# Optimization experiments

Hardware: AMD Instinct MI355X
Metric: run time of the kernel (lower is better)

Reference implementation:

```python
import jax, jax.numpy as jnp
import numpy as np

DIM = 2048
N_HEADS = 16
Q_RANK = 1536
KV_RANK = 512
D_NOPE = 128
D_ROPE = 64
D_V = 128
EPS = 1e-6
B, S = 2, 2048
ROPE_THETA = 10000.0


def rmsnorm(x, w, eps=EPS):
    return x * jax.lax.rsqrt(jnp.mean(x * x, axis=-1, keepdims=True) + eps) * w


def apply_rope(x):
    # x: [b, h, s, d] with d even; LLaMA-style interleaved pair rotation
    b, h, s, d = x.shape
    inv_freq = 1.0 / (ROPE_THETA ** (jnp.arange(0, d, 2, dtype=jnp.float32) / d))
    ang = jnp.arange(s, dtype=jnp.float32)[:, None] * inv_freq[None, :]  # [s, d/2]
    cos, sin = jnp.cos(ang), jnp.sin(ang)
    xr = x.reshape(b, h, s, d // 2, 2)
    x1, x2 = xr[..., 0], xr[..., 1]
    o1 = x1 * cos - x2 * sin
    o2 = x1 * sin + x2 * cos
    return jnp.stack([o1, o2], axis=-1).reshape(b, h, s, d)


def setup_inputs() -> dict:
    key = jax.random.key(0)
    ks = jax.random.split(key, 10)
    std = 0.02
    return {
        "x": jax.random.normal(ks[0], (B, S, DIM), dtype=jnp.float32),
        "wq_down": jax.random.normal(ks[1], (Q_RANK, DIM), dtype=jnp.float32) * std,
        "q_norm_w": jnp.ones((Q_RANK,), dtype=jnp.float32),
        "wq_up": jax.random.normal(ks[2], (N_HEADS * D_NOPE, Q_RANK), dtype=jnp.float32) * std,
        "wq_rope": jax.random.normal(ks[3], (N_HEADS * D_ROPE, Q_RANK), dtype=jnp.float32) * std,
        "wkv_down": jax.random.normal(ks[4], (KV_RANK, DIM), dtype=jnp.float32) * std,
        "kv_norm_w": jnp.ones((KV_RANK,), dtype=jnp.float32),
        "wkv_up": jax.random.normal(ks[5], (N_HEADS * (D_NOPE + D_V), KV_RANK), dtype=jnp.float32) * std,
        "wk_rope": jax.random.normal(ks[6], (D_ROPE, DIM), dtype=jnp.float32) * std,
        "wo": jax.random.normal(ks[7], (DIM, N_HEADS * D_V), dtype=jnp.float32) * std,
    }


def reference(x, wq_down, q_norm_w, wq_up, wq_rope, wkv_down, kv_norm_w, wkv_up, wk_rope, wo):
    bs, s, _ = x.shape
    # low-rank Q path
    q_c = rmsnorm(x @ wq_down.T, q_norm_w)                              # [b,s,qr]
    q_nope = (q_c @ wq_up.T).reshape(bs, s, N_HEADS, D_NOPE).transpose(0, 2, 1, 3)
    q_pe = (q_c @ wq_rope.T).reshape(bs, s, N_HEADS, D_ROPE).transpose(0, 2, 1, 3)
    # low-rank KV path
    kv_c = rmsnorm(x @ wkv_down.T, kv_norm_w)                           # [b,s,kvr]
    kv_up = (kv_c @ wkv_up.T).reshape(bs, s, N_HEADS, D_NOPE + D_V)
    k_nope = kv_up[..., :D_NOPE].transpose(0, 2, 1, 3)                  # [b,h,s,dn]
    v = kv_up[..., D_NOPE:].transpose(0, 2, 1, 3)                       # [b,h,s,dv]
    # shared rope key (1 head), broadcast across heads
    k_rope = (x @ wk_rope.T).reshape(bs, s, 1, D_ROPE).transpose(0, 2, 1, 3)  # [b,1,s,dr]
    q_pe = apply_rope(q_pe)
    k_rope = apply_rope(k_rope)
    q = jnp.concatenate([q_nope, q_pe], axis=-1)                        # [b,h,s,dn+dr]
    k = jnp.concatenate([k_nope, jnp.broadcast_to(k_rope, (bs, N_HEADS, s, D_ROPE))], axis=-1)
    scale = 1.0 / np.sqrt(D_NOPE + D_ROPE)
    scores = jnp.einsum('bhqd,bhkd->bhqk', q, k) * scale                # [b,h,s,s]
    causal = jnp.tril(jnp.ones((s, s), dtype=bool))
    scores = jnp.where(causal, scores, -jnp.inf)
    probs = jax.nn.softmax(scores, axis=-1)
    out = jnp.einsum('bhqk,bhkv->bhqv', probs, v)                       # [b,h,s,dv]
    out = out.transpose(0, 2, 1, 3).reshape(bs, s, N_HEADS * D_V)
    return out @ wo.T
```

## Files before the change

### kernel.cpp

```cpp
#include <hip/hip_runtime.h>
#include <stdint.h>

typedef _Float16 f16x8 __attribute__((ext_vector_type(8)));
typedef _Float16 f16x4 __attribute__((ext_vector_type(4)));
typedef float fx4 __attribute__((ext_vector_type(4)));

static constexpr int S_LEN = 2048;
static constexpr int BATCH = 2;
static constexpr int TOKENS = BATCH * S_LEN;
static constexpr int DIM = 2048;
static constexpr int NH = 16;
static constexpr int QR = 1536;
static constexpr int KVR = 512;
static constexpr int DN = 128;
static constexpr int DR = 64;
static constexpr int DV = 128;

__device__ __forceinline__ void async16(const _Float16* g, _Float16* lds_base_uniform) {
  __builtin_amdgcn_global_load_lds(
      (const __attribute__((address_space(1))) void*)g,
      (__attribute__((address_space(3))) void*)lds_base_uniform, 16, 0, 0);
}

__device__ __forceinline__ void bar() {
  asm volatile("" ::: "memory");
  __builtin_amdgcn_s_barrier();
  asm volatile("" ::: "memory");
}
#define VMWAIT(n) asm volatile("s_waitcnt vmcnt(" #n ")" ::: "memory")

#define ROR16(x, ctrl) \
  __uint_as_float(__builtin_amdgcn_update_dpp(__float_as_uint(x), __float_as_uint(x), \
                                              (ctrl), 0xF, 0xF, false))

__device__ __forceinline__ void sincos_rev(float ang, float* sn, float* cs) {
  float rev = ang * 0.15915494309189535f;
  rev -= floorf(rev);
  *sn = __builtin_amdgcn_sinf(rev);
  *cs = __builtin_amdgcn_cosf(rev);
}

struct CvtSegs {
  const float* src[8];
  _Float16* dst[8];
  int n4[8];
  int cum[9];
};
__global__ __launch_bounds__(256) void cvt_all(CvtSegs s) {
  const int b = blockIdx.x;
  int seg = 0;
#pragma unroll
  for (int k = 0; k < 7; ++k) seg += (b >= s.cum[seg + 1]) ? 1 : 0;
  const int i = (b - s.cum[seg]) * 256 + threadIdx.x;
  if (i >= s.n4[seg]) return;
  fx4 v = *(const fx4*)(s.src[seg] + (size_t)i * 4);
  f16x4 o;
  o[0] = (_Float16)v[0]; o[1] = (_Float16)v[1];
  o[2] = (_Float16)v[2]; o[3] = (_Float16)v[3];
  *(f16x4*)(s.dst[seg] + (size_t)i * 4) = o;
}

template <int MODE>
__global__ __launch_bounds__(256) void gemm_nt(const _Float16* __restrict__ A,
                                               const _Float16* __restrict__ W,
                                               void* __restrict__ C0v,
                                               void* __restrict__ C1v,
                                               void* __restrict__ C2v,
                                               int M, int N, int K) {
  __shared__ __attribute__((aligned(16))) _Float16 As[3][128 * 32];
  __shared__ __attribute__((aligned(16))) _Float16 Ws[3][128 * 32];
  const int tid = threadIdx.x;
  const int lane = tid & 63;
  const int wave = tid >> 6;
  const int wr = (wave >> 1) * 64;
  const int wc = (wave & 1) * 64;
  const int m16 = lane & 15;
  const int quad = lane >> 4;
  const int m0 = blockIdx.y * 128;
  const int n0 = blockIdx.x * 128;

  auto stage = [&](int buf, int k0) {
#pragma unroll
    for (int p = 0; p < 2; ++p) {
      const int cb = p * 256 + wave * 64;
      const int ch = cb + lane;
      const int r = ch >> 2;
      const int c8 = (ch & 3) * 8;
      async16(A + (size_t)(m0 + r) * K + k0 + c8, &As[buf][cb * 8]);
      async16(W + (size_t)(n0 + r) * K + k0 + c8, &Ws[buf][cb * 8]);
    }
  };

  const fx4 fz = {0.f, 0.f, 0.f, 0.f};
  fx4 acc[4][4];
#pragma unroll
  for (int i = 0; i < 4; ++i)
#pragma unroll
    for (int j = 0; j < 4; ++j) acc[i][j] = fz;

  const int nkt = K >> 5;
  stage(0, 0);
  stage(1, 32);
  int cur = 0;
  for (int kt = 0; kt < nkt; ++kt) {
    if (kt + 1 < nkt) { VMWAIT(4); } else { VMWAIT(0); }
    bar();
    if (kt + 2 < nkt) {
      int b2 = cur + 2; if (b2 >= 3) b2 -= 3;
      stage(b2, (kt + 2) * 32);
    }
    const _Float16* as = As[cur];
    const _Float16* ws = Ws[cur];
    f16x8 af[4], wf[4];
#pragma unroll
    for (int i = 0; i < 4; ++i)
      af[i] = *(const f16x8*)(&as[(wr + i * 16 + m16) * 32 + quad * 8]);
#pragma unroll
    for (int j = 0; j < 4; ++j)
      wf[j] = *(const f16x8*)(&ws[(wc + j * 16 + m16) * 32 + quad * 8]);
#pragma unroll
    for (int i = 0; i < 4; ++i)
#pragma unroll
      for (int j = 0; j < 4; ++j)
        acc[i][j] = __builtin_amdgcn_mfma_f32_16x16x32_f16(af[i], wf[j], acc[i][j], 0, 0, 0);
    if (++cur == 3) cur = 0;
  }

#pragma unroll
  for (int j = 0; j < 4; ++j) {
    const int col = n0 + wc + j * 16 + m16;
    if (MODE == 5) {
#pragma unroll
      for (int i = 0; i < 4; ++i)
#pragma unroll
        for (int r = 0; r < 4; ++r) {
          const size_t row = (size_t)(m0 + wr + i * 16 + quad * 4 + r);
          const _Float16 v = (_Float16)acc[i][j][r];
          if (col < 1536)      ((_Float16*)C0v)[row * 1536 + col] = v;
          else if (col < 2048) ((_Float16*)C1v)[row * 512 + col - 1536] = v;
          else if (col < 2112) ((_Float16*)C2v)[row * 64 + col - 2048] = v;
        }
    } else {
      if (col < N) {
#pragma unroll
        for (int i = 0; i < 4; ++i)
#pragma unroll
          for (int r = 0; r < 4; ++r) {
            const size_t row = (size_t)(m0 + wr + i * 16 + quad * 4 + r);
            ((float*)C0v)[row * N + col] = acc[i][j][r];
          }
      }
    }
  }
}

__global__ __launch_bounds__(256) void gemm_up(
    const _Float16* __restrict__ qc, const _Float16* __restrict__ wqu,
    const _Float16* __restrict__ kvc, const _Float16* __restrict__ wkvu,
    _Float16* __restrict__ qnope, _Float16* __restrict__ qpe,
    _Float16* __restrict__ knope, _Float16* __restrict__ vT) {
  __shared__ __attribute__((aligned(16))) _Float16 As[3][128 * 32];
  __shared__ __attribute__((aligned(16))) _Float16 Ws[3][128 * 32];
  const int tid = threadIdx.x;
  const int lane = tid & 63;
  const int wave = tid >> 6;
  const int wr = (wave >> 1) * 64;
  const int wc = (wave & 1) * 64;
  const int m16 = lane & 15;
  const int quad = lane >> 4;
  const int m0 = blockIdx.y * 128;
  const bool isq = (blockIdx.x < 24);
  const int n0 = (isq ? blockIdx.x : blockIdx.x - 24) * 128;
  const _Float16* A = isq ? qc : kvc;
  const _Float16* W = isq ? wqu : wkvu;
  const int K = isq ? QR : KVR;

  auto stage = [&](int buf, int k0) {
#pragma unroll
    for (int p = 0; p < 2; ++p) {
      const int cb = p * 256 + wave * 64;
      const int ch = cb + lane;
      const int r = ch >> 2;
      const int c8 = (ch & 3) * 8;
      async16(A + (size_t)(m0 + r) * K + k0 + c8, &As[buf][cb * 8]);
      async16(W + (size_t)(n0 + r) * K + k0 + c8, &Ws[buf][cb * 8]);
    }
  };

  const fx4 fz = {0.f, 0.f, 0.f, 0.f};
  fx4 acc[4][4];
#pragma unroll
  for (int i = 0; i < 4; ++i)
#pragma unroll
    for (int j = 0; j < 4; ++j) acc[i][j] = fz;

  const int nkt = K >> 5;
  stage(0, 0);
  stage(1, 32);
  int cur = 0;
  for (int kt = 0; kt < nkt; ++kt) {
    if (kt + 1 < nkt) { VMWAIT(4); } else { VMWAIT(0); }
    bar();
    if (kt + 2 < nkt) {
      int b2 = cur + 2; if (b2 >= 3) b2 -= 3;
      stage(b2, (kt + 2) * 32);
    }
    const _Float16* as = As[cur];
    const _Float16* ws = Ws[cur];
    f16x8 af[4], wf[4];
#pragma unroll
    for (int i = 0; i < 4; ++i)
      af[i] = *(const f16x8*)(&as[(wr + i * 16 + m16) * 32 + quad * 8]);
#pragma unroll
    for (int j = 0; j < 4; ++j)
      wf[j] = *(const f16x8*)(&ws[(wc + j * 16 + m16) * 32 + quad * 8]);
#pragma unroll
    for (int i = 0; i < 4; ++i)
#pragma unroll
      for (int j = 0; j < 4; ++j)
        acc[i][j] = __builtin_amdgcn_mfma_f32_16x16x32_f16(af[i], wf[j], acc[i][j], 0, 0, 0);
    if (++cur == 3) cur = 0;
  }

#pragma unroll
  for (int j = 0; j < 4; ++j) {
    const int col = n0 + wc + j * 16 + m16;
    if (isq) {
#pragma unroll
      for (int i = 0; i < 4; ++i)
#pragma unroll
        for (int r = 0; r < 4; ++r) {
          const size_t row = (size_t)(m0 + wr + i * 16 + quad * 4 + r);
          if (col < 2048) qnope[row * 2048 + col] = (_Float16)acc[i][j][r];
          else qpe[row * 1024 + col - 2048] = (_Float16)acc[i][j][r];
        }
    } else {
      const int head = col >> 8;
      const int sub = col & 255;
      if (sub < 128) {
#pragma unroll
        for (int i = 0; i < 4; ++i)
#pragma unroll
          for (int r = 0; r < 4; ++r)
            knope[(size_t)(m0 + wr + i * 16 + quad * 4 + r) * 2048 + head * 128 + sub] =
                (_Float16)acc[i][j][r];
      } else {
        const int dv = sub - 128;
#pragma unroll
        for (int i = 0; i < 4; ++i) {
          f16x4 v;
#pragma unroll
          for (int r = 0; r < 4; ++r) v[r] = (_Float16)acc[i][j][r];
          *(f16x4*)(&vT[(size_t)(head * 128 + dv) * TOKENS + m0 + wr + i * 16 + quad * 4]) = v;
        }
      }
    }
  }
}

__global__ __launch_bounds__(256) void rms_rope(_Float16* __restrict__ qc,
                                                const float* __restrict__ qw,
                                                _Float16* __restrict__ kvc,
                                                const float* __restrict__ kvw,
                                                _Float16* __restrict__ kr) {
  const int bid = blockIdx.x;
  if (bid < 2 * TOKENS) {
    const bool isq = bid < TOKENS;
    const int row = isq ? bid : bid - TOKENS;
    const int NC = isq ? QR : KVR;
    _Float16* p = (isq ? qc : kvc) + (size_t)row * NC;
    const float* w = isq ? qw : kvw;
    float ss = 0.f;
    for (int c = threadIdx.x; c < NC; c += 256) {
      const float v = (float)p[c];
      ss += v * v;
    }
#pragma unroll
    for (int d = 1; d < 64; d <<= 1) ss += __shfl_xor(ss, d);
    __shared__ float red[4];
    if ((threadIdx.x & 63) == 0) red[threadIdx.x >> 6] = ss;
    __syncthreads();
    const float rs = rsqrtf((red[0] + red[1] + red[2] + red[3]) / (float)NC + 1e-6f);
    for (int c = threadIdx.x; c < NC; c += 256)
      p[c] = (_Float16)((float)p[c] * rs * w[c]);
  } else {
    const int idx = (bid - 2 * TOKENS) * 256 + threadIdx.x;
    const int t = idx >> 5;
    const int i = idx & 31;
    const int s = t & (S_LEN - 1);
    const float fr = exp2f(-(float)i * 0.4152410118609203f);
    const float ang = (float)s * fr;
    float sn, cs;
    sincos_rev(ang, &sn, &cs);
    const size_t base = (size_t)t * DR + 2 * i;
    const float x1 = (float)kr[base];
    const float x2 = (float)kr[base + 1];
    kr[base] = (_Float16)(x1 * cs - x2 * sn);
    kr[base + 1] = (_Float16)(x1 * sn + x2 * cs);
  }
}

__global__ __launch_bounds__(256, 2) void mla_attn(
    const _Float16* __restrict__ qn,
    const _Float16* __restrict__ qp,
    const _Float16* __restrict__ kn,
    const _Float16* __restrict__ kr,
    const _Float16* __restrict__ vT,
    _Float16* __restrict__ out)
{
  __shared__ __attribute__((aligned(16))) _Float16 Ks[2][768 * 8];
  __shared__ __attribute__((aligned(16))) _Float16 Vs[2][512 * 8];
  __shared__ __attribute__((aligned(16))) _Float16 Ps[4][16][40];

  const int bid = blockIdx.x;
  const int j = bid >> 5;
  const int bh = bid & 31;
  const int b = bh >> 4;
  const int h = bh & 15;
  const int q32 = 31 - j;
  const int qb = q32 * 64;
  const int tok0 = b * S_LEN;

  const int tid = threadIdx.x;
  const int lane = tid & 63;
  const int wave = tid >> 6;
  const int m16 = lane & 15;
  const int quad = lane >> 4;
  const int R0 = qb + wave * 16;

  auto stageKV = [&](int buf, int kbase) {
#pragma unroll
    for (int jj = 0; jj < 3; ++jj) {
      const int i = wave * 3 + jj;
      const int ch = i * 2 + (lane >> 5);
      const int key = lane & 31;
      const _Float16* g = (ch < 16)
          ? kn + (size_t)(tok0 + kbase + key) * 2048 + h * 128 + ch * 8
          : kr + (size_t)(tok0 + kbase + key) * 64 + (ch - 16) * 8;
      async16(g, &Ks[buf][i * 512]);
    }
#pragma unroll
    for (int jj = 0; jj < 2; ++jj) {
      const int i = wave * 2 + jj;
      const int p = i * 64 + lane;
      const int L = p ^ ((p >> 3) & 3);
      const int dv = L >> 2;
      const int qc = L & 3;
      async16(vT + (size_t)(h * 128 + dv) * TOKENS + tok0 + kbase + qc * 8,
              &Vs[buf][i * 512]);
    }
  };

  const float scale2 = 0.07216878364870323f * 1.4426950408889634f;
  const fx4 fz = {0.f, 0.f, 0.f, 0.f};

  f16x8 qf[6];
  {
    const int srow = qb + wave * 16 + m16;
    const size_t t = (size_t)(tok0 + srow);
#pragma unroll
    for (int kk = 0; kk < 4; ++kk)
      qf[kk] = *(const f16x8*)(qn + t * 2048 + h * 128 + kk * 32 + quad * 8);
#pragma unroll
    for (int kk = 0; kk < 2; ++kk) {
      f16x8 v = *(const f16x8*)(qp + t * 1024 + h * 64 + kk * 32 + quad * 8);
      f16x8 o;
      const int i0 = kk * 16 + quad * 4;
#pragma unroll
      for (int jj = 0; jj < 4; ++jj) {
        const float ang = (float)srow * exp2f(-(float)(i0 + jj) * 0.4152410118609203f);
        float sn, cs;
        sincos_rev(ang, &sn, &cs);
        const float x1 = (float)v[2 * jj], x2 = (float)v[2 * jj + 1];
        o[2 * jj]     = (_Float16)(x1 * cs - x2 * sn);
        o[2 * jj + 1] = (_Float16)(x1 * sn + x2 * cs);
      }
      qf[4 + kk] = o;
    }
  }

  fx4 oacc[9];
#pragma unroll
  for (int n = 0; n < 9; ++n) oacc[n] = fz;
  float mst[4];
#pragma unroll
  for (int r = 0; r < 4; ++r) mst[r] = -3.0e38f;
  f16x8 vones;
#pragma unroll
  for (int e = 0; e < 8; ++e) vones[e] = (_Float16)1.0f;

  const int nkt = (qb >> 5) + 2;

  stageKV(0, 0);
  for (int kt = 0; kt < nkt; ++kt) {
    const int kbase = kt * 32;
    __syncthreads();
    if (kt + 1 < nkt) stageKV((kt + 1) & 1, kbase + 32);

    const bool live = (kbase <= R0 + 15);
    if (!live) continue;
    const _Float16* ks = Ks[kt & 1];
    const _Float16* vs = Vs[kt & 1];

    fx4 sc[2];
    sc[0] = fz; sc[1] = fz;
    __builtin_amdgcn_s_setprio(1);
#pragma unroll
    for (int kk = 0; kk < 6; ++kk) {
#pragma unroll
      for (int n = 0; n < 2; ++n) {
        f16x8 kf = *(const f16x8*)(&ks[(kk * 128 + quad * 32 + n * 16 + m16) * 8]);
        sc[n] = __builtin_amdgcn_mfma_f32_16x16x32_f16(qf[kk], kf, sc[n], 0, 0, 0);
      }
    }
    __builtin_amdgcn_s_setprio(0);

    f16x8 vf[8];
#pragma unroll
    for (int n8 = 0; n8 < 8; ++n8) {
      const int c0 = (n8 * 16 + m16) * 4 + quad;
      vf[n8] = *(const f16x8*)(&vs[(c0 ^ ((c0 >> 3) & 3)) * 8]);
    }

    const bool needmask = (kbase + 31 > R0);
    float alpha[4];
    bool any_upd = false;
#pragma unroll
    for (int r = 0; r < 4; ++r) {
      float v0 = sc[0][r] * scale2;
      float v1 = sc[1][r] * scale2;
      if (needmask) {
        const int qrow = R0 + quad * 4 + r;
        if (kbase + m16 > qrow)      v0 = -3.0e38f;
        if (kbase + 16 + m16 > qrow) v1 = -3.0e38f;
      }
      const float pre = fmaxf(v0, v1);
      float al = 1.0f;
      if (__any(pre > mst[r] + 10.0f)) {
        float mx = pre;
        mx = fmaxf(mx, ROR16(mx, 0x128));
        mx = fmaxf(mx, ROR16(mx, 0x124));
        mx = fmaxf(mx, ROR16(mx, 0x122));
        mx = fmaxf(mx, ROR16(mx, 0x121));
        const float mn = fmaxf(mst[r], mx);
        al = exp2f(mst[r] - mn);
        mst[r] = mn;
        any_upd = true;
      }
      alpha[r] = al;
      const float p0 = exp2f(v0 - mst[r]);
      const float p1 = exp2f(v1 - mst[r]);
      _Float16* pr = &Ps[wave][quad * 4 + r][0];
      pr[m16] = (_Float16)p0;
      pr[16 + m16] = (_Float16)p1;
    }
    if (any_upd) {
#pragma unroll
      for (int n8 = 0; n8 < 9; ++n8)
#pragma unroll
        for (int r = 0; r < 4; ++r) oacc[n8][r] *= alpha[r];
    }

    f16x8 pf = *(const f16x8*)(&Ps[wave][m16][quad * 8]);
    __builtin_amdgcn_s_setprio(1);
#pragma unroll
    for (int n8 = 0; n8 < 8; ++n8)
      oacc[n8] = __builtin_amdgcn_mfma_f32_16x16x32_f16(pf, vf[n8], oacc[n8], 0, 0, 0);
    oacc[8] = __builtin_amdgcn_mfma_f32_16x16x32_f16(pf, vones, oacc[8], 0, 0, 0);
    __builtin_amdgcn_s_setprio(0);
  }

  float inv[4];
#pragma unroll
  for (int r = 0; r < 4; ++r) inv[r] = 1.0f / oacc[8][r];
#pragma unroll
  for (int n8 = 0; n8 < 8; ++n8) {
#pragma unroll
    for (int r = 0; r < 4; ++r) {
      const size_t t = (size_t)(tok0 + qb + wave * 16 + quad * 4 + r);
      out[t * 2048 + h * 128 + n8 * 16 + m16] = (_Float16)(oacc[n8][r] * inv[r]);
    }
  }
}

extern "C" void kernel_launch(void* const* d_in, const int* in_sizes, int n_in,
                              void* d_out, int out_size, void* d_ws, size_t ws_size,
                              hipStream_t stream) {
  const float* x         = (const float*)d_in[0];
  const float* wq_down   = (const float*)d_in[1];
  const float* q_norm_w  = (const float*)d_in[2];
  const float* wq_up     = (const float*)d_in[3];
  const float* wq_rope   = (const float*)d_in[4];
  const float* wkv_down  = (const float*)d_in[5];
  const float* kv_norm_w = (const float*)d_in[6];
  const float* wkv_up    = (const float*)d_in[7];
  const float* wk_rope   = (const float*)d_in[8];
  const float* wo        = (const float*)d_in[9];
  float* out = (float*)d_out;

  char* ws = (char*)d_ws;
  size_t off = 0;
  auto alloc = [&](size_t bytes) {
    char* p = ws + off;
    off += (bytes + 255) & ~(size_t)255;
    return p;
  };
  _Float16* x_h     = (_Float16*)alloc((size_t)TOKENS * DIM * 2);
  _Float16* wA_h    = (_Float16*)alloc((size_t)2176 * DIM * 2);
  _Float16* wquqr_h = (_Float16*)alloc((size_t)3072 * QR * 2);
  _Float16* wkvu_h  = (_Float16*)alloc((size_t)NH * 256 * KVR * 2);
  _Float16* wo_h    = (_Float16*)alloc((size_t)DIM * NH * DV * 2);
  _Float16* qc_h    = (_Float16*)alloc((size_t)TOKENS * QR * 2);
  _Float16* kvc_h   = (_Float16*)alloc((size_t)TOKENS * KVR * 2);
  _Float16* qnope_h = (_Float16*)alloc((size_t)TOKENS * 2048 * 2);
  _Float16* qpe_h   = (_Float16*)alloc((size_t)TOKENS * 1024 * 2);
  _Float16* knope_h = (_Float16*)alloc((size_t)TOKENS * 2048 * 2);
  _Float16* vT_h    = (_Float16*)alloc((size_t)2048 * TOKENS * 2);
  _Float16* krope_h = (_Float16*)alloc((size_t)TOKENS * DR * 2);
  _Float16* attn_h  = (_Float16*)alloc((size_t)TOKENS * 2048 * 2);

  CvtSegs cs;
  const float* srcs[8] = {x, wq_down, wq_up, wq_rope, wkv_down, wk_rope, wkv_up, wo};
  _Float16* dsts[8] = {x_h, wA_h, wquqr_h, wquqr_h + (size_t)2048 * QR,
                       wA_h + (size_t)1536 * DIM, wA_h + (size_t)2048 * DIM,
                       wkvu_h, wo_h};
  const size_t ns[8] = {(size_t)TOKENS * DIM, (size_t)QR * DIM, (size_t)2048 * QR,
                        (size_t)1024 * QR, (size_t)KVR * DIM, (size_t)DR * DIM,
                        (size_t)NH * 256 * KVR, (size_t)DIM * NH * DV};
  int cum = 0;
  for (int i = 0; i < 8; ++i) {
    cs.src[i] = srcs[i];
    cs.dst[i] = dsts[i];
    cs.n4[i] = (int)(ns[i] / 4);
    cs.cum[i] = cum;
    cum += (cs.n4[i] + 255) / 256;
  }
  cs.cum[8] = cum;
  cvt_all<<<dim3(cum), 256, 0, stream>>>(cs);

  const unsigned gm = TOKENS / 128;

  gemm_nt<5><<<dim3(17, gm), 256, 0, stream>>>(x_h, wA_h, qc_h, kvc_h, krope_h,
                                               TOKENS, 2112, DIM);
  rms_rope<<<dim3(2 * TOKENS + TOKENS * 32 / 256), 256, 0, stream>>>(
      qc_h, q_norm_w, kvc_h, kv_norm_w, krope_h);
  gemm_up<<<dim3(24 + 32, gm), 256, 0, stream>>>(qc_h, wquqr_h, kvc_h, wkvu_h,
                                                 qnope_h, qpe_h, knope_h, vT_h);
  mla_attn<<<dim3(1024), 256, 0, stream>>>(qnope_h, qpe_h, knope_h, krope_h, vT_h, attn_h);
  gemm_nt<1><<<dim3(16, gm), 256, 0, stream>>>(attn_h, wo_h, out, nullptr, nullptr,
                                               TOKENS, DIM, NH * DV);
}
```

Measured before the change: 475.8 us.

## Fuse RMSNorm and k-rope into GEMM epilogues, enlarge attention blocks

Removes the separate rms_rope kernel. The norm weights are folded into the up-projection weights during fp16 conversion, and the per-row rsqrt is computed from the A-operand fragments inside gemm_up. The shared-key rope is applied in the down-projection GEMM epilogue. The attention kernel moves to 512-thread blocks covering 128 query rows, halving the grid. This saves a launch and a read-modify-write pass over qc/kvc, at the cost of extra ALU work in the GEMM main loop and a different occupancy profile for attention.

```diff
diff --git a/kernel.cpp b/kernel.cpp
--- a/kernel.cpp
+++ b/kernel.cpp
@@ -43,6 +43,8 @@
 struct CvtSegs {
   const float* src[8];
   _Float16* dst[8];
+  const float* nw[8];
+  int nmod[8];
   int n4[8];
   int cum[9];
 };
@@ -54,6 +56,11 @@
   const int i = (b - s.cum[seg]) * 256 + threadIdx.x;
   if (i >= s.n4[seg]) return;
   fx4 v = *(const fx4*)(s.src[seg] + (size_t)i * 4);
+  if (s.nw[seg]) {
+    const int c0 = (int)(((size_t)i * 4) % (size_t)s.nmod[seg]);
+    fx4 wv = *(const fx4*)(s.nw[seg] + c0);
+    v[0] *= wv[0]; v[1] *= wv[1]; v[2] *= wv[2]; v[3] *= wv[3];
+  }
   f16x4 o;
   o[0] = (_Float16)v[0]; o[1] = (_Float16)v[1];
   o[2] = (_Float16)v[2]; o[3] = (_Float16)v[3];
@@ -130,16 +137,35 @@
   for (int j = 0; j < 4; ++j) {
     const int col = n0 + wc + j * 16 + m16;
     if (MODE == 5) {
-#pragma unroll
-      for (int i = 0; i < 4; ++i)
-#pragma unroll
-        for (int r = 0; r < 4; ++r) {
-          const size_t row = (size_t)(m0 + wr + i * 16 + quad * 4 + r);
-          const _Float16 v = (_Float16)acc[i][j][r];
-          if (col < 1536)      ((_Float16*)C0v)[row * 1536 + col] = v;
-          else if (col < 2048) ((_Float16*)C1v)[row * 512 + col - 1536] = v;
-          else if (col < 2112) ((_Float16*)C2v)[row * 64 + col - 2048] = v;
-        }
+      if (col < 2048) {
+#pragma unroll
+        for (int i = 0; i < 4; ++i)
+#pragma unroll
+          for (int r = 0; r < 4; ++r) {
+            const size_t row = (size_t)(m0 + wr + i * 16 + quad * 4 + r);
+            const _Float16 v = (_Float16)acc[i][j][r];
+            if (col < 1536) ((_Float16*)C0v)[row * 1536 + col] = v;
+            else            ((_Float16*)C1v)[row * 512 + col - 1536] = v;
+          }
+      } else if (col < 2112) {
+        const int d = col - 2048;
+        const int pidx = d >> 1;
+        const bool odd = (d & 1);
+        const float fr = exp2f(-(float)pidx * 0.4152410118609203f);
+#pragma unroll
+        for (int i = 0; i < 4; ++i)
+#pragma unroll
+          for (int r = 0; r < 4; ++r) {
+            const size_t row = (size_t)(m0 + wr + i * 16 + quad * 4 + r);
+            const int spos = (int)(row & (S_LEN - 1));
+            float sn, cs;
+            sincos_rev((float)spos * fr, &sn, &cs);
+            const float own = acc[i][j][r];
+            const float oth = __shfl_xor(own, 1);
+            const float res = odd ? (oth * sn + own * cs) : (own * cs - oth * sn);
+            ((_Float16*)C2v)[row * 64 + d] = (_Float16)res;
+          }
+      }
     } else {
       if (col < N) {
 #pragma unroll
@@ -193,6 +219,7 @@
   for (int i = 0; i < 4; ++i)
 #pragma unroll
     for (int j = 0; j < 4; ++j) acc[i][j] = fz;
+  float ssq[4] = {0.f, 0.f, 0.f, 0.f};
 
   const int nkt = K >> 5;
   stage(0, 0);
@@ -219,7 +246,26 @@
 #pragma unroll
       for (int j = 0; j < 4; ++j)
         acc[i][j] = __builtin_amdgcn_mfma_f32_16x16x32_f16(af[i], wf[j], acc[i][j], 0, 0, 0);
+#pragma unroll
+    for (int i = 0; i < 4; ++i) {
+      float s0 = 0.f;
+#pragma unroll
+      for (int e = 0; e < 8; ++e) { const float xv = (float)af[i][e]; s0 += xv * xv; }
+      ssq[i] += s0;
+    }
     if (++cur == 3) cur = 0;
+  }
+
+  const float invK = 1.0f / (float)K;
+  float rsq[4][4];
+#pragma unroll
+  for (int i = 0; i < 4; ++i) {
+    float ss = ssq[i];
+    ss += __shfl_xor(ss, 16);
+    ss += __shfl_xor(ss, 32);
+    const float rv = rsqrtf(ss * invK + 1e-6f);
+#pragma unroll
+    for (int r = 0; r < 4; ++r) rsq[i][r] = __shfl(rv, quad * 4 + r);
   }
 
 #pragma unroll
@@ -231,8 +277,9 @@
 #pragma unroll
         for (int r = 0; r < 4; ++r) {
           const size_t row = (size_t)(m0 + wr + i * 16 + quad * 4 + r);
-          if (col < 2048) qnope[row * 2048 + col] = (_Float16)acc[i][j][r];
-          else qpe[row * 1024 + col - 2048] = (_Float16)acc[i][j][r];
+          const _Float16 v = (_Float16)(acc[i][j][r] * rsq[i][r]);
+          if (col < 2048) qnope[row * 2048 + col] = v;
+          else qpe[row * 1024 + col - 2048] = v;
         }
     } else {
       const int head = col >> 8;
@@ -243,14 +290,14 @@
 #pragma unroll
           for (int r = 0; r < 4; ++r)
             knope[(size_t)(m0 + wr + i * 16 + quad * 4 + r) * 2048 + head * 128 + sub] =
-                (_Float16)acc[i][j][r];
+                (_Float16)(acc[i][j][r] * rsq[i][r]);
       } else {
         const int dv = sub - 128;
 #pragma unroll
         for (int i = 0; i < 4; ++i) {
           f16x4 v;
 #pragma unroll
-          for (int r = 0; r < 4; ++r) v[r] = (_Float16)acc[i][j][r];
+          for (int r = 0; r < 4; ++r) v[r] = (_Float16)(acc[i][j][r] * rsq[i][r]);
           *(f16x4*)(&vT[(size_t)(head * 128 + dv) * TOKENS + m0 + wr + i * 16 + quad * 4]) = v;
         }
       }
@@ -258,49 +305,7 @@
   }
 }
 
-__global__ __launch_bounds__(256) void rms_rope(_Float16* __restrict__ qc,
-                                                const float* __restrict__ qw,
-                                                _Float16* __restrict__ kvc,
-                                                const float* __restrict__ kvw,
-                                                _Float16* __restrict__ kr) {
-  const int bid = blockIdx.x;
-  if (bid < 2 * TOKENS) {
-    const bool isq = bid < TOKENS;
-    const int row = isq ? bid : bid - TOKENS;
-    const int NC = isq ? QR : KVR;
-    _Float16* p = (isq ? qc : kvc) + (size_t)row * NC;
-    const float* w = isq ? qw : kvw;
-    float ss = 0.f;
-    for (int c = threadIdx.x; c < NC; c += 256) {
-      const float v = (float)p[c];
-      ss += v * v;
-    }
-#pragma unroll
-    for (int d = 1; d < 64; d <<= 1) ss += __shfl_xor(ss, d);
-    __shared__ float red[4];
-    if ((threadIdx.x & 63) == 0) red[threadIdx.x >> 6] = ss;
-    __syncthreads();
-    const float rs = rsqrtf((red[0] + red[1] + red[2] + red[3]) / (float)NC + 1e-6f);
-    for (int c = threadIdx.x; c < NC; c += 256)
-      p[c] = (_Float16)((float)p[c] * rs * w[c]);
-  } else {
-    const int idx = (bid - 2 * TOKENS) * 256 + threadIdx.x;
-    const int t = idx >> 5;
-    const int i = idx & 31;
-    const int s = t & (S_LEN - 1);
-    const float fr = exp2f(-(float)i * 0.4152410118609203f);
-    const float ang = (float)s * fr;
-    float sn, cs;
-    sincos_rev(ang, &sn, &cs);
-    const size_t base = (size_t)t * DR + 2 * i;
-    const float x1 = (float)kr[base];
-    const float x2 = (float)kr[base + 1];
-    kr[base] = (_Float16)(x1 * cs - x2 * sn);
-    kr[base + 1] = (_Float16)(x1 * sn + x2 * cs);
-  }
-}
-
-__global__ __launch_bounds__(256, 2) void mla_attn(
+__global__ __launch_bounds__(512, 2) void mla_attn(
     const _Float16* __restrict__ qn,
     const _Float16* __restrict__ qp,
     const _Float16* __restrict__ kn,
@@ -310,15 +315,15 @@
 {
   __shared__ __attribute__((aligned(16))) _Float16 Ks[2][768 * 8];
   __shared__ __attribute__((aligned(16))) _Float16 Vs[2][512 * 8];
-  __shared__ __attribute__((aligned(16))) _Float16 Ps[4][16][40];
+  __shared__ __attribute__((aligned(16))) _Float16 Ps[8][16][40];
 
   const int bid = blockIdx.x;
   const int j = bid >> 5;
   const int bh = bid & 31;
   const int b = bh >> 4;
   const int h = bh & 15;
-  const int q32 = 31 - j;
-  const int qb = q32 * 64;
+  const int q16 = 15 - j;
+  const int qb = q16 * 128;
   const int tok0 = b * S_LEN;
 
   const int tid = threadIdx.x;
@@ -331,23 +336,23 @@
   auto stageKV = [&](int buf, int kbase) {
 #pragma unroll
     for (int jj = 0; jj < 3; ++jj) {
-      const int i = wave * 3 + jj;
-      const int ch = i * 2 + (lane >> 5);
-      const int key = lane & 31;
-      const _Float16* g = (ch < 16)
-          ? kn + (size_t)(tok0 + kbase + key) * 2048 + h * 128 + ch * 8
-          : kr + (size_t)(tok0 + kbase + key) * 64 + (ch - 16) * 8;
-      async16(g, &Ks[buf][i * 512]);
-    }
-#pragma unroll
-    for (int jj = 0; jj < 2; ++jj) {
-      const int i = wave * 2 + jj;
-      const int p = i * 64 + lane;
-      const int L = p ^ ((p >> 3) & 3);
-      const int dv = L >> 2;
-      const int qc = L & 3;
-      async16(vT + (size_t)(h * 128 + dv) * TOKENS + tok0 + kbase + qc * 8,
-              &Vs[buf][i * 512]);
+      const int idx = wave * 3 + jj;
+      if (idx < 12) {
+        const int ch = idx * 2 + (lane >> 5);
+        const int key = lane & 31;
+        const _Float16* g = (ch < 16)
+            ? kn + (size_t)(tok0 + kbase + key) * 2048 + h * 128 + ch * 8
+            : kr + (size_t)(tok0 + kbase + key) * 64 + (ch - 16) * 8;
+        async16(g, &Ks[buf][idx * 512]);
+      } else if (idx < 20) {
+        const int iv = idx - 12;
+        const int p = iv * 64 + lane;
+        const int L = p ^ ((p >> 3) & 3);
+        const int dv = L >> 2;
+        const int qcc = L & 3;
+        async16(vT + (size_t)(h * 128 + dv) * TOKENS + tok0 + kbase + qcc * 8,
+                &Vs[buf][iv * 512]);
+      }
     }
   };
 
@@ -389,7 +394,7 @@
 #pragma unroll
   for (int e = 0; e < 8; ++e) vones[e] = (_Float16)1.0f;
 
-  const int nkt = (qb >> 5) + 2;
+  const int nkt = (qb >> 5) + 4;
 
   stageKV(0, 0);
   for (int kt = 0; kt < nkt; ++kt) {
@@ -524,6 +529,9 @@
   _Float16* dsts[8] = {x_h, wA_h, wquqr_h, wquqr_h + (size_t)2048 * QR,
                        wA_h + (size_t)1536 * DIM, wA_h + (size_t)2048 * DIM,
                        wkvu_h, wo_h};
+  const float* nws[8] = {nullptr, nullptr, q_norm_w, q_norm_w, nullptr, nullptr,
+                         kv_norm_w, nullptr};
+  const int nmods[8] = {4, 4, QR, QR, 4, 4, KVR, 4};
   const size_t ns[8] = {(size_t)TOKENS * DIM, (size_t)QR * DIM, (size_t)2048 * QR,
                         (size_t)1024 * QR, (size_t)KVR * DIM, (size_t)DR * DIM,
                         (size_t)NH * 256 * KVR, (size_t)DIM * NH * DV};
@@ -531,6 +539,8 @@
   for (int i = 0; i < 8; ++i) {
     cs.src[i] = srcs[i];
     cs.dst[i] = dsts[i];
+    cs.nw[i] = nws[i];
+    cs.nmod[i] = nmods[i];
     cs.n4[i] = (int)(ns[i] / 4);
     cs.cum[i] = cum;
     cum += (cs.n4[i] + 255) / 256;
@@ -542,11 +552,9 @@
 
   gemm_nt<5><<<dim3(17, gm), 256, 0, stream>>>(x_h, wA_h, qc_h, kvc_h, krope_h,
                                                TOKENS, 2112, DIM);
-  rms_rope<<<dim3(2 * TOKENS + TOKENS * 32 / 256), 256, 0, stream>>>(
-      qc_h, q_norm_w, kvc_h, kv_norm_w, krope_h);
   gemm_up<<<dim3(24 + 32, gm), 256, 0, stream>>>(qc_h, wquqr_h, kvc_h, wkvu_h,
                                                  qnope_h, qpe_h, knope_h, vT_h);
-  mla_attn<<<dim3(1024), 256, 0, stream>>>(qnope_h, qpe_h, knope_h, krope_h, vT_h, attn_h);
+  mla_attn<<<dim3(512), 512, 0, stream>>>(qnope_h, qpe_h, knope_h, krope_h, vT_h, attn_h);
   gemm_nt<1><<<dim3(16, gm), 256, 0, stream>>>(attn_h, wo_h, out, nullptr, nullptr,
                                                TOKENS, DIM, NH * DV);
 }
```

New measurement: 472.4 us. No clear change (-0.7%).
